# Optimization experiments

Hardware: AMD Instinct MI355X
Metric: run time of the kernel (lower is better)

The kernel has to match this reference:

```python
import jax, jax.numpy as jnp
import numpy as np

HIDDEN = 2048
N_HEADS = 16
N_KV_HEADS = 4
HEAD_DIM = HIDDEN // N_HEADS  # 128
BATCH = 1
SEQ = 2048
EPS = 1e-6


def _rms_norm(x, scale, eps=EPS):
    var = jnp.mean(jnp.square(x), axis=-1, keepdims=True)
    return x * jax.lax.rsqrt(var + eps) * scale


def _rotate_half(x):
    x1, x2 = jnp.split(x, 2, axis=-1)
    return jnp.concatenate((-x2, x1), axis=-1)


def setup_inputs() -> dict:
    key = jax.random.key(0)
    ks = jax.random.split(key, 8)
    hidden_states = jax.random.normal(ks[0], (BATCH, SEQ, HIDDEN), dtype=jnp.float32)
    # causal mask, broadcastable over [B, H, S, S]
    attention_mask = jnp.tril(jnp.ones((SEQ, SEQ), dtype=bool))[None, None, :, :]
    # standard RoPE tables, broadcastable against [B, S, H, D]
    inv_freq = 1.0 / (10000.0 ** (np.arange(0, HEAD_DIM, 2, dtype=np.float32) / HEAD_DIM))
    t = np.arange(SEQ, dtype=np.float32)
    freqs = np.outer(t, inv_freq)                      # [S, D/2]
    emb = np.concatenate([freqs, freqs], axis=-1)      # [S, D]
    cos = jnp.asarray(np.cos(emb))[:, None, :]         # [S, 1, D]
    sin = jnp.asarray(np.sin(emb))[:, None, :]
    s = 1.0 / np.sqrt(HIDDEN)
    Wq = jax.random.normal(ks[1], (HIDDEN, N_HEADS * HEAD_DIM), dtype=jnp.float32) * s
    Wk = jax.random.normal(ks[2], (HIDDEN, N_KV_HEADS * HEAD_DIM), dtype=jnp.float32) * s
    Wv = jax.random.normal(ks[3], (HIDDEN, N_KV_HEADS * HEAD_DIM), dtype=jnp.float32) * s
    Wo = jax.random.normal(ks[4], (HIDDEN, HIDDEN), dtype=jnp.float32) * s
    q_norm_scale = jnp.ones((HEAD_DIM,), dtype=jnp.float32)
    k_norm_scale = jnp.ones((HEAD_DIM,), dtype=jnp.float32)
    last_norm_scale = jnp.ones((HIDDEN,), dtype=jnp.float32)
    return {
        "hidden_states": hidden_states,
        "cos": cos,
        "sin": sin,
        "Wq": Wq,
        "Wk": Wk,
        "Wv": Wv,
        "Wo": Wo,
        "q_norm_scale": q_norm_scale,
        "k_norm_scale": k_norm_scale,
        "last_norm_scale": last_norm_scale,
        "attention_mask": attention_mask,
    }


def reference(hidden_states, cos, sin, Wq, Wk, Wv, Wo,
              q_norm_scale, k_norm_scale, last_norm_scale, attention_mask):
    B, S, _ = hidden_states.shape
    q = (hidden_states @ Wq).reshape(B, S, N_HEADS, HEAD_DIM)
    k = (hidden_states @ Wk).reshape(B, S, N_KV_HEADS, HEAD_DIM)
    v = (hidden_states @ Wv).reshape(B, S, N_KV_HEADS, HEAD_DIM)
    # per-head RMSNorm on Q/K
    q = _rms_norm(q, q_norm_scale)
    k = _rms_norm(k, k_norm_scale)
    # RoPE (cos/sin broadcast [S,1,D] -> [B,S,H,D])
    q = q * cos + _rotate_half(q) * sin
    k = k * cos + _rotate_half(k) * sin
    # GQA expansion
    groups = N_HEADS // N_KV_HEADS
    if groups > 1:
        k = jnp.repeat(k, groups, axis=2)
        v = jnp.repeat(v, groups, axis=2)
    out = jax.nn.dot_product_attention(q, k, v, mask=attention_mask)  # [B,S,H,D]
    out = out.reshape(B, S, HIDDEN) @ Wo
    return _rms_norm(out, last_norm_scale)
```

## Files before the change

### kernel.cpp

```cpp
#include <hip/hip_runtime.h>

typedef unsigned short u16;
typedef unsigned int u32;

#define S 2048
#define HID 2048
#define NH 16
#define NKV 4
#define D 128
#define QKVP 3072
#define QSCALE (0.08838834764831845f * 1.4426950408889634f)
#define NEG_INF -3.0e38f

typedef __attribute__((ext_vector_type(8))) short short8;
typedef __attribute__((ext_vector_type(4))) float f32x4;

__device__ __forceinline__ float bf2f(u16 u) {
  union { u32 i; float f; } c; c.i = ((u32)u) << 16; return c.f;
}
__device__ __forceinline__ u16 f2bf(float f) {
  union { float f; u32 i; } c; c.f = f;
  u32 x = c.i;
  u32 r = x + 0x7fffu + ((x >> 16) & 1u);
  return (u16)(r >> 16);
}

#if __has_builtin(__builtin_amdgcn_exp2f)
__device__ __forceinline__ float exp2_hw(float x) { return __builtin_amdgcn_exp2f(x); }
#else
__device__ __forceinline__ float exp2_hw(float x) { return exp2f(x); }
#endif

__device__ __forceinline__ u32 cvt_pk_bf16(float a, float b) {
  u32 r;
  asm("v_cvt_pk_bf16_f32 %0, %1, %2" : "=v"(r) : "v"(a), "v"(b));
  return r;
}

__device__ __forceinline__ void gload16(const u16* g, u16* l) {
  __builtin_amdgcn_global_load_lds(
      (const __attribute__((address_space(1))) u32*)g,
      (__attribute__((address_space(3))) u32*)l, 16, 0, 0);
}

__global__ __launch_bounds__(256) void k_cvt(const float* __restrict__ src,
                                             u16* __restrict__ dst) {
  int i = (blockIdx.x * 256 + threadIdx.x) * 8;
  float4 v0 = *(const float4*)(src + i);
  float4 v1 = *(const float4*)(src + i + 4);
  ushort4 w0, w1;
  w0.x = f2bf(v0.x); w0.y = f2bf(v0.y); w0.z = f2bf(v0.z); w0.w = f2bf(v0.w);
  w1.x = f2bf(v1.x); w1.y = f2bf(v1.y); w1.z = f2bf(v1.z); w1.w = f2bf(v1.w);
  *(ushort4*)(dst + i) = w0;
  *(ushort4*)(dst + i + 4) = w1;
}

__device__ __forceinline__ void transpose_body(const float* __restrict__ src,
                                               u16* __restrict__ dst,
                                               int N, int K, int nt, int kt,
                                               int t) {
  __shared__ float T[64][65];
#pragma unroll
  for (int it = 0; it < 4; ++it) {
    int r = it * 16 + (t >> 4), c = (t & 15) * 4;
    float4 v = *(const float4*)(src + (size_t)(kt + r) * N + nt + c);
    T[r][c] = v.x; T[r][c + 1] = v.y; T[r][c + 2] = v.z; T[r][c + 3] = v.w;
  }
  __syncthreads();
#pragma unroll
  for (int it = 0; it < 2; ++it) {
    int n = it * 32 + (t >> 3), k8 = (t & 7) * 8;
    ushort4 w0, w1;
    w0.x = f2bf(T[k8 + 0][n]); w0.y = f2bf(T[k8 + 1][n]);
    w0.z = f2bf(T[k8 + 2][n]); w0.w = f2bf(T[k8 + 3][n]);
    w1.x = f2bf(T[k8 + 4][n]); w1.y = f2bf(T[k8 + 5][n]);
    w1.z = f2bf(T[k8 + 6][n]); w1.w = f2bf(T[k8 + 7][n]);
    *(ushort4*)(dst + (size_t)(nt + n) * K + kt + k8) = w0;
    *(ushort4*)(dst + (size_t)(nt + n) * K + kt + k8 + 4) = w1;
  }
}

__global__ __launch_bounds__(256) void k_transpose(const float* __restrict__ src,
                                                   u16* __restrict__ dst,
                                                   int N, int K) {
  transpose_body(src, dst, N, K, blockIdx.x * 64, blockIdx.y * 64, threadIdx.x);
}

__global__ __launch_bounds__(256) void k_transpose_qkv(const float* __restrict__ Wq,
                                                       const float* __restrict__ Wk,
                                                       const float* __restrict__ Wv,
                                                       u16* __restrict__ WT) {
  const int bx = blockIdx.x;
  const float* src; u16* dst; int N, nt;
  if (bx < 32)      { src = Wq; dst = WT;                    N = 2048; nt = bx * 64; }
  else if (bx < 40) { src = Wk; dst = WT + 2048ull * 2048;   N = 512;  nt = (bx - 32) * 64; }
  else              { src = Wv; dst = WT + 2560ull * 2048;   N = 512;  nt = (bx - 40) * 64; }
  transpose_body(src, dst, N, 2048, nt, blockIdx.y * 64, threadIdx.x);
}

__global__ __launch_bounds__(256) void k_vt(const u16* __restrict__ QKV,
                                            u16* __restrict__ Vt) {
  __shared__ u16 T[64][66];
  const int t = threadIdx.x;
  const int s0 = blockIdx.x * 64, d0 = blockIdx.y * 64;
#pragma unroll
  for (int it = 0; it < 4; ++it) {
    int r = it * 16 + (t >> 4), c = (t & 15) * 4;
    ushort4 v = *(const ushort4*)(QKV + (size_t)(s0 + r) * QKVP + 2560 + d0 + c);
    T[r][c] = v.x; T[r][c + 1] = v.y; T[r][c + 2] = v.z; T[r][c + 3] = v.w;
  }
  __syncthreads();
#pragma unroll
  for (int it = 0; it < 4; ++it) {
    int dd = it * 16 + (t >> 4), sc = (t & 15) * 4;
    ushort4 w;
    w.x = T[sc + 0][dd]; w.y = T[sc + 1][dd];
    w.z = T[sc + 2][dd]; w.w = T[sc + 3][dd];
    *(ushort4*)(Vt + (size_t)(d0 + dd) * S + s0 + sc) = w;
  }
}

__global__ __launch_bounds__(256) void k_gemm_mfma(const u16* __restrict__ A,
                                                   const u16* __restrict__ BT,
                                                   void* __restrict__ Cout,
                                                   int N, int K, int out_bf16) {
  __shared__ __align__(16) u16 As[2][128 * 32];
  __shared__ __align__(16) u16 Bs[2][128 * 32];
  const int t = threadIdx.x, w = t >> 6, lane = t & 63;
  const int l15 = lane & 15, quad = lane >> 4;
  const int m0 = blockIdx.y * 128, n0 = blockIdx.x * 128;
  const int wr = w >> 1, wc = w & 1;

  const int sr = w * 16 + (lane >> 2);
  const int sk8 = (lane & 3) * 8;
  const u16* Ag0 = A + (size_t)(m0 + sr) * K + sk8;
  const u16* Ag1 = A + (size_t)(m0 + 64 + sr) * K + sk8;
  const u16* Bg0 = BT + (size_t)(n0 + sr) * K + sk8;
  const u16* Bg1 = BT + (size_t)(n0 + 64 + sr) * K + sk8;

  f32x4 acc[4][4];
#pragma unroll
  for (int i = 0; i < 4; ++i)
#pragma unroll
    for (int j = 0; j < 4; ++j) acc[i][j] = (f32x4){0.f, 0.f, 0.f, 0.f};

  auto STAGE = [&](int k0, int b) {
    gload16(Ag0 + k0, &As[b][w * 512]);
    gload16(Ag1 + k0, &As[b][2048 + w * 512]);
    gload16(Bg0 + k0, &Bs[b][w * 512]);
    gload16(Bg1 + k0, &Bs[b][2048 + w * 512]);
  };

  STAGE(0, 0);
  __syncthreads();
  int cur = 0;
  for (int k0 = 0; k0 < K; k0 += 32) {
    if (k0 + 32 < K) STAGE(k0 + 32, cur ^ 1);

    short8 af[4], bf[4];
#pragma unroll
    for (int i = 0; i < 4; ++i)
      af[i] = *(const short8*)&As[cur][(wr * 64 + i * 16 + l15) * 32 + quad * 8];
#pragma unroll
    for (int j = 0; j < 4; ++j)
      bf[j] = *(const short8*)&Bs[cur][(wc * 64 + j * 16 + l15) * 32 + quad * 8];
#pragma unroll
    for (int i = 0; i < 4; ++i)
#pragma unroll
      for (int j = 0; j < 4; ++j)
        acc[i][j] = __builtin_amdgcn_mfma_f32_16x16x32_bf16(af[i], bf[j], acc[i][j], 0, 0, 0);

    __syncthreads();
    cur ^= 1;
  }

  if (out_bf16) {
    u16* C = (u16*)Cout;
#pragma unroll
    for (int i = 0; i < 4; ++i)
#pragma unroll
      for (int j = 0; j < 4; ++j) {
        int col = n0 + wc * 64 + j * 16 + l15;
#pragma unroll
        for (int r = 0; r < 4; ++r)
          C[(size_t)(m0 + wr * 64 + i * 16 + quad * 4 + r) * N + col] = f2bf(acc[i][j][r]);
      }
  } else {
    float* C = (float*)Cout;
#pragma unroll
    for (int i = 0; i < 4; ++i)
#pragma unroll
      for (int j = 0; j < 4; ++j) {
        int col = n0 + wc * 64 + j * 16 + l15;
#pragma unroll
        for (int r = 0; r < 4; ++r)
          C[(size_t)(m0 + wr * 64 + i * 16 + quad * 4 + r) * N + col] = acc[i][j][r];
      }
  }
}

__global__ __launch_bounds__(128) void k_norm_rope(u16* __restrict__ QKV,
                                                   const float* __restrict__ qsc,
                                                   const float* __restrict__ ksc,
                                                   const float* __restrict__ cosp,
                                                   const float* __restrict__ sinp) {
  const int s = blockIdx.x, hh = blockIdx.y, d = threadIdx.x;
  u16* row; const float* sc; float scale;
  if (hh < NH) { row = QKV + (size_t)s * QKVP + hh * D;            sc = qsc; scale = QSCALE; }
  else         { row = QKV + (size_t)s * QKVP + 2048 + (hh - NH) * D; sc = ksc; scale = 1.0f; }
  float x = bf2f(row[d]);
  float v = x * x;
#pragma unroll
  for (int o = 32; o; o >>= 1) v += __shfl_xor(v, o, 64);
  __shared__ float red[2];
  if ((d & 63) == 0) red[d >> 6] = v;
  __syncthreads();
  float var = (red[0] + red[1]) * (1.0f / 128.0f);
  float rinv = rsqrtf(var + 1e-6f) * scale;
  float xn = x * rinv * sc[d];
  __shared__ float sh[D];
  sh[d] = xn;
  __syncthreads();
  float rot = (d < 64) ? -sh[d + 64] : sh[d - 64];
  row[d] = f2bf(xn * cosp[s * D + d] + rot * sinp[s * D + d]);
}

#define KP 128
#define PTP 72

__global__ __launch_bounds__(256) void k_flash(const u16* __restrict__ QKV,
                                               const u16* __restrict__ Vt,
                                               u16* __restrict__ O) {
  const int h = blockIdx.y, g = h >> 2;
  const int qt = (h < 8) ? (31 - (int)blockIdx.x) : (int)blockIdx.x;
  const int t = threadIdx.x;
  const int w = t >> 6, lane = t & 63, l15 = lane & 15, quad = lane >> 4;

  __shared__ __align__(16) u16 Klds[2][64 * KP];
  __shared__ __align__(16) u16 Vlds[128 * 64];
  __shared__ __align__(16) u16 Pt[4][16 * PTP];

  const int qbase = qt * 64 + w * 16;
  const int qrow = qbase + l15;

  short8 qf[4];
  {
    const u16* qp = QKV + (size_t)qrow * QKVP + h * D + quad * 8;
#pragma unroll
    for (int c = 0; c < 4; ++c) qf[c] = *(const short8*)(qp + c * 32);
  }

  float m = NEG_INF, l = 0.f;
  f32x4 oacc[8];
#pragma unroll
  for (int nc = 0; nc < 8; ++nc) oacc[nc] = (f32x4){0.f, 0.f, 0.f, 0.f};

  const int nt = qt + 1;
  const int dd = t >> 3, cc = t & 7;

  auto KLOAD = [&](int j0, int b) {
#pragma unroll
    for (int it = 0; it < 4; ++it) {
      int rl = w * 16 + it * 4 + quad;
      int gchunk = (lane & 15) ^ (rl & 7);
      const u16* gp = QKV + (size_t)(j0 + rl) * QKVP + 2048 + g * D + gchunk * 8;
      gload16(gp, &Klds[b][(w * 16 + it * 4) * KP]);
    }
  };
  auto VLOAD = [&](int j0, uint4* vr) {
#pragma unroll
    for (int it = 0; it < 4; ++it)
      vr[it] = *(const uint4*)(Vt + (size_t)(g * D + dd + it * 32) * S + j0 + cc * 8);
  };
  auto VWRITE = [&](uint4* vr) {
#pragma unroll
    for (int it = 0; it < 4; ++it) {
      int d = dd + it * 32;
      *(uint4*)&Vlds[d * 64 + ((cc ^ (d & 7)) * 8)] = vr[it];
    }
  };
  auto COMPUTE = [&](int jt, int b) {
    const int j0 = jt * 64;
    f32x4 sa[4];
#pragma unroll
    for (int sub = 0; sub < 4; ++sub) {
      f32x4 acc = {0.f, 0.f, 0.f, 0.f};
#pragma unroll
      for (int c = 0; c < 4; ++c) {
        int ch = (c * 4 + quad) ^ (l15 & 7);
        short8 kf = *(const short8*)&Klds[b][(sub * 16 + l15) * KP + ch * 8];
        acc = __builtin_amdgcn_mfma_f32_16x16x32_bf16(kf, qf[c], acc, 0, 0, 0);
      }
      sa[sub] = acc;
    }
    if (jt == nt - 1) {
#pragma unroll
      for (int sub = 0; sub < 4; ++sub) {
        int keyb = j0 + sub * 16 + quad * 4;
#pragma unroll
        for (int r = 0; r < 4; ++r)
          if (keyb + r > qrow) sa[sub][r] = NEG_INF;
      }
    }
    float tmax = sa[0][0];
#pragma unroll
    for (int sub = 0; sub < 4; ++sub)
#pragma unroll
      for (int r = 0; r < 4; ++r) tmax = fmaxf(tmax, sa[sub][r]);
    tmax = fmaxf(tmax, __shfl_xor(tmax, 16, 64));
    tmax = fmaxf(tmax, __shfl_xor(tmax, 32, 64));
    float mn = fmaxf(m, tmax);
    float alpha = exp2_hw(m - mn);
    m = mn;
    float rs = 0.f;
#pragma unroll
    for (int sub = 0; sub < 4; ++sub) {
      float p0 = exp2_hw(sa[sub][0] - m);
      float p1 = exp2_hw(sa[sub][1] - m);
      float p2 = exp2_hw(sa[sub][2] - m);
      float p3 = exp2_hw(sa[sub][3] - m);
      rs += (p0 + p1) + (p2 + p3);
      u32 lo = cvt_pk_bf16(p0, p1);
      u32 hi = cvt_pk_bf16(p2, p3);
      *(uint2*)&Pt[w][l15 * PTP + sub * 16 + quad * 4] = make_uint2(lo, hi);
    }
    rs += __shfl_xor(rs, 16, 64);
    rs += __shfl_xor(rs, 32, 64);
    l = l * alpha + rs;
#pragma unroll
    for (int nc = 0; nc < 8; ++nc) {
      oacc[nc][0] *= alpha; oacc[nc][1] *= alpha;
      oacc[nc][2] *= alpha; oacc[nc][3] *= alpha;
    }
#pragma unroll
    for (int kc = 0; kc < 2; ++kc) {
      short8 pf = *(const short8*)&Pt[w][l15 * PTP + kc * 32 + quad * 8];
#pragma unroll
      for (int nc = 0; nc < 8; ++nc) {
        int d = nc * 16 + l15;
        short8 vf = *(const short8*)&Vlds[d * 64 + (((kc * 4 + quad) ^ (d & 7)) * 8)];
        oacc[nc] = __builtin_amdgcn_mfma_f32_16x16x32_bf16(vf, pf, oacc[nc], 0, 0, 0);
      }
    }
  };

  uint4 vrA[4], vrB[4];
  KLOAD(0, 0);
  VLOAD(0, vrA);
  for (int jt = 0; jt < nt; jt += 2) {
    __syncthreads();
    VWRITE(vrA);
    __syncthreads();
    if (jt + 1 < nt) { KLOAD((jt + 1) * 64, 1); VLOAD((jt + 1) * 64, vrB); }
    COMPUTE(jt, 0);
    if (jt + 1 < nt) {
      __syncthreads();
      VWRITE(vrB);
      __syncthreads();
      if (jt + 2 < nt) { KLOAD((jt + 2) * 64, 0); VLOAD((jt + 2) * 64, vrA); }
      COMPUTE(jt + 1, 1);
    }
  }

  float inv = 1.0f / l;
  u16* orow = O + (size_t)qrow * HID + h * D;
#pragma unroll
  for (int nc = 0; nc < 8; ++nc) {
    ushort4 wv;
    wv.x = f2bf(oacc[nc][0] * inv); wv.y = f2bf(oacc[nc][1] * inv);
    wv.z = f2bf(oacc[nc][2] * inv); wv.w = f2bf(oacc[nc][3] * inv);
    *(ushort4*)(orow + nc * 16 + quad * 4) = wv;
  }
}

__device__ __forceinline__ float blockSum256(float v, float* red, int t) {
#pragma unroll
  for (int o = 32; o; o >>= 1) v += __shfl_xor(v, o, 64);
  if ((t & 63) == 0) red[t >> 6] = v;
  __syncthreads();
  v = red[0] + red[1] + red[2] + red[3];
  __syncthreads();
  return v;
}

__global__ __launch_bounds__(256) void k_fnorm(const float* __restrict__ X,
                                               const float* __restrict__ sc,
                                               float* __restrict__ out) {
  const int s = blockIdx.x, t = threadIdx.x;
  const float* row = X + (size_t)s * HID;
  float4 r0 = *(const float4*)(row + t * 8);
  float4 r1 = *(const float4*)(row + t * 8 + 4);
  float x[8] = {r0.x, r0.y, r0.z, r0.w, r1.x, r1.y, r1.z, r1.w};
  float ss = 0.f;
#pragma unroll
  for (int ii = 0; ii < 8; ++ii) ss += x[ii] * x[ii];
  __shared__ float red[4];
  float tot = blockSum256(ss, red, t);
  float rinv = rsqrtf(tot * (1.0f / 2048.0f) + 1e-6f);
  float4 s0 = *(const float4*)(sc + t * 8);
  float4 s1 = *(const float4*)(sc + t * 8 + 4);
  float4 w0 = make_float4(x[0] * rinv * s0.x, x[1] * rinv * s0.y,
                          x[2] * rinv * s0.z, x[3] * rinv * s0.w);
  float4 w1 = make_float4(x[4] * rinv * s1.x, x[5] * rinv * s1.y,
                          x[6] * rinv * s1.z, x[7] * rinv * s1.w);
  *(float4*)(out + (size_t)s * HID + t * 8) = w0;
  *(float4*)(out + (size_t)s * HID + t * 8 + 4) = w1;
}

extern "C" void kernel_launch(void* const* d_in, const int* in_sizes, int n_in,
                              void* d_out, int out_size, void* d_ws, size_t ws_size,
                              hipStream_t stream) {
  const float* hidden = (const float*)d_in[0];
  const float* cosp   = (const float*)d_in[1];
  const float* sinp   = (const float*)d_in[2];
  const float* Wq     = (const float*)d_in[3];
  const float* Wk     = (const float*)d_in[4];
  const float* Wv     = (const float*)d_in[5];
  const float* Wo     = (const float*)d_in[6];
  const float* qsc    = (const float*)d_in[7];
  const float* ksc    = (const float*)d_in[8];
  const float* lsc    = (const float*)d_in[9];
  float* out = (float*)d_out;

  char* ws = (char*)d_ws;
  u16*   Hb  = (u16*)(ws);
  u16*   WoT = (u16*)(ws);
  u16*   WT  = (u16*)(ws + (8ull << 20));
  u16*   An  = (u16*)(ws + (8ull << 20));
  u16*   QKV = (u16*)(ws + (20ull << 20));
  float* Ob  = (float*)(ws + (20ull << 20));
  u16*   Vtb = (u16*)(ws + (32ull << 20));

  k_cvt<<<S * HID / (256 * 8), 256, 0, stream>>>(hidden, Hb);
  k_transpose_qkv<<<dim3(48, 32), 256, 0, stream>>>(Wq, Wk, Wv, WT);
  k_gemm_mfma<<<dim3(24, 16), 256, 0, stream>>>(Hb, WT, QKV, QKVP, 2048, 1);
  k_transpose<<<dim3(32, 32), 256, 0, stream>>>(Wo, WoT, 2048, 2048);
  k_norm_rope<<<dim3(S, NH + NKV), 128, 0, stream>>>(QKV, qsc, ksc, cosp, sinp);
  k_vt<<<dim3(32, 8), 256, 0, stream>>>(QKV, Vtb);
  k_flash<<<dim3(32, NH), 256, 0, stream>>>(QKV, Vtb, An);
  k_gemm_mfma<<<dim3(16, 16), 256, 0, stream>>>(An, WoT, Ob, 2048, 2048, 0);
  k_fnorm<<<S, 256, 0, stream>>>(Ob, lsc, out);
}
```

Before: 321.9 us.

## Load V fragments directly from global into registers and skip rescaling lazily

The flash kernel no longer stages V through LDS. Each wave reads its V^T MFMA fragments straight from global memory into registers, split into two halves issued around the QK^T MFMAs, and the loop drops to one barrier per tile. The online-softmax rescale of the output accumulator is also skipped unless the running max grows by more than 8 (in log2 units) for some lane. This removes LDS writes and barriers, but every wave now fetches the full V tile from global/L2 on its own (4x redundant reads per block) and register pressure rises.

```diff
diff --git a/kernel.cpp b/kernel.cpp
--- a/kernel.cpp
+++ b/kernel.cpp
@@ -237,7 +237,6 @@
   const int w = t >> 6, lane = t & 63, l15 = lane & 15, quad = lane >> 4;
 
   __shared__ __align__(16) u16 Klds[2][64 * KP];
-  __shared__ __align__(16) u16 Vlds[128 * 64];
   __shared__ __align__(16) u16 Pt[4][16 * PTP];
 
   const int qbase = qt * 64 + w * 16;
@@ -256,7 +255,6 @@
   for (int nc = 0; nc < 8; ++nc) oacc[nc] = (f32x4){0.f, 0.f, 0.f, 0.f};
 
   const int nt = qt + 1;
-  const int dd = t >> 3, cc = t & 7;
 
   auto KLOAD = [&](int j0, int b) {
 #pragma unroll
@@ -267,20 +265,21 @@
       gload16(gp, &Klds[b][(w * 16 + it * 4) * KP]);
     }
   };
-  auto VLOAD = [&](int j0, uint4* vr) {
-#pragma unroll
-    for (int it = 0; it < 4; ++it)
-      vr[it] = *(const uint4*)(Vt + (size_t)(g * D + dd + it * 32) * S + j0 + cc * 8);
-  };
-  auto VWRITE = [&](uint4* vr) {
-#pragma unroll
-    for (int it = 0; it < 4; ++it) {
-      int d = dd + it * 32;
-      *(uint4*)&Vlds[d * 64 + ((cc ^ (d & 7)) * 8)] = vr[it];
-    }
-  };
-  auto COMPUTE = [&](int jt, int b) {
+
+  KLOAD(0, 0);
+  for (int jt = 0; jt < nt; ++jt) {
+    const int b = jt & 1;
+    __syncthreads();
+    if (jt + 1 < nt) KLOAD((jt + 1) * 64, b ^ 1);
+
     const int j0 = jt * 64;
+    const u16* vbase = Vt + (size_t)g * D * S + j0;
+
+    short8 vf0[8];
+#pragma unroll
+    for (int nc = 0; nc < 8; ++nc)
+      vf0[nc] = *(const short8*)(vbase + (size_t)(nc * 16 + l15) * S + quad * 8);
+
     f32x4 sa[4];
 #pragma unroll
     for (int sub = 0; sub < 4; ++sub) {
@@ -293,6 +292,12 @@
       }
       sa[sub] = acc;
     }
+
+    short8 vf1[8];
+#pragma unroll
+    for (int nc = 0; nc < 8; ++nc)
+      vf1[nc] = *(const short8*)(vbase + (size_t)(nc * 16 + l15) * S + 32 + quad * 8);
+
     if (jt == nt - 1) {
 #pragma unroll
       for (int sub = 0; sub < 4; ++sub) {
@@ -302,6 +307,7 @@
           if (keyb + r > qrow) sa[sub][r] = NEG_INF;
       }
     }
+
     float tmax = sa[0][0];
 #pragma unroll
     for (int sub = 0; sub < 4; ++sub)
@@ -309,9 +315,17 @@
       for (int r = 0; r < 4; ++r) tmax = fmaxf(tmax, sa[sub][r]);
     tmax = fmaxf(tmax, __shfl_xor(tmax, 16, 64));
     tmax = fmaxf(tmax, __shfl_xor(tmax, 32, 64));
-    float mn = fmaxf(m, tmax);
-    float alpha = exp2_hw(m - mn);
-    m = mn;
+    if (jt == 0 || !__all(tmax - m <= 8.f)) {
+      float mn = (jt == 0) ? tmax : fmaxf(m, tmax);
+      float alpha = (jt == 0) ? 0.f : exp2_hw(m - mn);
+      m = mn;
+      l *= alpha;
+#pragma unroll
+      for (int nc = 0; nc < 8; ++nc) {
+        oacc[nc][0] *= alpha; oacc[nc][1] *= alpha;
+        oacc[nc][2] *= alpha; oacc[nc][3] *= alpha;
+      }
+    }
     float rs = 0.f;
 #pragma unroll
     for (int sub = 0; sub < 4; ++sub) {
@@ -326,39 +340,17 @@
     }
     rs += __shfl_xor(rs, 16, 64);
     rs += __shfl_xor(rs, 32, 64);
-    l = l * alpha + rs;
-#pragma unroll
-    for (int nc = 0; nc < 8; ++nc) {
-      oacc[nc][0] *= alpha; oacc[nc][1] *= alpha;
-      oacc[nc][2] *= alpha; oacc[nc][3] *= alpha;
-    }
-#pragma unroll
-    for (int kc = 0; kc < 2; ++kc) {
-      short8 pf = *(const short8*)&Pt[w][l15 * PTP + kc * 32 + quad * 8];
-#pragma unroll
-      for (int nc = 0; nc < 8; ++nc) {
-        int d = nc * 16 + l15;
-        short8 vf = *(const short8*)&Vlds[d * 64 + (((kc * 4 + quad) ^ (d & 7)) * 8)];
-        oacc[nc] = __builtin_amdgcn_mfma_f32_16x16x32_bf16(vf, pf, oacc[nc], 0, 0, 0);
-      }
-    }
-  };
-
-  uint4 vrA[4], vrB[4];
-  KLOAD(0, 0);
-  VLOAD(0, vrA);
-  for (int jt = 0; jt < nt; jt += 2) {
-    __syncthreads();
-    VWRITE(vrA);
-    __syncthreads();
-    if (jt + 1 < nt) { KLOAD((jt + 1) * 64, 1); VLOAD((jt + 1) * 64, vrB); }
-    COMPUTE(jt, 0);
-    if (jt + 1 < nt) {
-      __syncthreads();
-      VWRITE(vrB);
-      __syncthreads();
-      if (jt + 2 < nt) { KLOAD((jt + 2) * 64, 0); VLOAD((jt + 2) * 64, vrA); }
-      COMPUTE(jt + 1, 1);
+    l += rs;
+
+    {
+      short8 pf0 = *(const short8*)&Pt[w][l15 * PTP + quad * 8];
+      short8 pf1 = *(const short8*)&Pt[w][l15 * PTP + 32 + quad * 8];
+#pragma unroll
+      for (int nc = 0; nc < 8; ++nc)
+        oacc[nc] = __builtin_amdgcn_mfma_f32_16x16x32_bf16(vf0[nc], pf0, oacc[nc], 0, 0, 0);
+#pragma unroll
+      for (int nc = 0; nc < 8; ++nc)
+        oacc[nc] = __builtin_amdgcn_mfma_f32_16x16x32_bf16(vf1[nc], pf1, oacc[nc], 0, 0, 0);
     }
   }
 
```

New measurement: 333.0 us. 3.5% more time.

## Retile GEMM to 128x64 blocks with K=64 stages and XOR-swizzled LDS

Applied to the files above, without the earlier changes.

The MFMA GEMM moves from 128x128 output tiles with a K step of 32 to 128x64 tiles with a K step of 64. LDS chunks are XOR-swizzled to avoid bank conflicts, and each wave now owns 32 rows across the full 64 columns. The grid doubles so the QKV and output projections launch more blocks across the CUs, and there are half as many barriers per K. In exchange, each block reuses fewer A/B loads, so global traffic per output goes up, and each thread holds fewer accumulators.

```diff
diff --git a/kernel.cpp b/kernel.cpp
--- a/kernel.cpp
+++ b/kernel.cpp
@@ -124,51 +124,56 @@
                                                    const u16* __restrict__ BT,
                                                    void* __restrict__ Cout,
                                                    int N, int K, int out_bf16) {
-  __shared__ __align__(16) u16 As[2][128 * 32];
-  __shared__ __align__(16) u16 Bs[2][128 * 32];
+  __shared__ __align__(16) u16 As[2][128 * 64];
+  __shared__ __align__(16) u16 Bs[2][64 * 64];
   const int t = threadIdx.x, w = t >> 6, lane = t & 63;
   const int l15 = lane & 15, quad = lane >> 4;
-  const int m0 = blockIdx.y * 128, n0 = blockIdx.x * 128;
-  const int wr = w >> 1, wc = w & 1;
-
-  const int sr = w * 16 + (lane >> 2);
-  const int sk8 = (lane & 3) * 8;
-  const u16* Ag0 = A + (size_t)(m0 + sr) * K + sk8;
-  const u16* Ag1 = A + (size_t)(m0 + 64 + sr) * K + sk8;
-  const u16* Bg0 = BT + (size_t)(n0 + sr) * K + sk8;
-  const u16* Bg1 = BT + (size_t)(n0 + 64 + sr) * K + sk8;
-
-  f32x4 acc[4][4];
-#pragma unroll
-  for (int i = 0; i < 4; ++i)
+  const int m0 = blockIdx.y * 128, n0 = blockIdx.x * 64;
+
+  const int srow = lane >> 3;
+  const int schunk = (lane & 7) ^ srow;
+  const u16* Agb = A + (size_t)(m0 + w * 8 + srow) * K + schunk * 8;
+  const u16* Bgb = BT + (size_t)(n0 + w * 8 + srow) * K + schunk * 8;
+
+  f32x4 acc[2][4];
+#pragma unroll
+  for (int i = 0; i < 2; ++i)
 #pragma unroll
     for (int j = 0; j < 4; ++j) acc[i][j] = (f32x4){0.f, 0.f, 0.f, 0.f};
 
   auto STAGE = [&](int k0, int b) {
-    gload16(Ag0 + k0, &As[b][w * 512]);
-    gload16(Ag1 + k0, &As[b][2048 + w * 512]);
-    gload16(Bg0 + k0, &Bs[b][w * 512]);
-    gload16(Bg1 + k0, &Bs[b][2048 + w * 512]);
+#pragma unroll
+    for (int it = 0; it < 4; ++it)
+      gload16(Agb + (size_t)it * 32 * K + k0, &As[b][(w * 8 + it * 32) * 64]);
+#pragma unroll
+    for (int it = 0; it < 2; ++it)
+      gload16(Bgb + (size_t)it * 32 * K + k0, &Bs[b][(w * 8 + it * 32) * 64]);
   };
 
   STAGE(0, 0);
   __syncthreads();
   int cur = 0;
-  for (int k0 = 0; k0 < K; k0 += 32) {
-    if (k0 + 32 < K) STAGE(k0 + 32, cur ^ 1);
-
-    short8 af[4], bf[4];
-#pragma unroll
-    for (int i = 0; i < 4; ++i)
-      af[i] = *(const short8*)&As[cur][(wr * 64 + i * 16 + l15) * 32 + quad * 8];
-#pragma unroll
-    for (int j = 0; j < 4; ++j)
-      bf[j] = *(const short8*)&Bs[cur][(wc * 64 + j * 16 + l15) * 32 + quad * 8];
-#pragma unroll
-    for (int i = 0; i < 4; ++i)
+  for (int k0 = 0; k0 < K; k0 += 64) {
+    if (k0 + 64 < K) STAGE(k0 + 64, cur ^ 1);
+
+    short8 af[2][2], bf[4][2];
+#pragma unroll
+    for (int k2 = 0; k2 < 2; ++k2) {
+      int ch = (k2 * 4 + quad) ^ (l15 & 7);
+#pragma unroll
+      for (int i = 0; i < 2; ++i)
+        af[i][k2] = *(const short8*)&As[cur][(w * 32 + i * 16 + l15) * 64 + ch * 8];
 #pragma unroll
       for (int j = 0; j < 4; ++j)
-        acc[i][j] = __builtin_amdgcn_mfma_f32_16x16x32_bf16(af[i], bf[j], acc[i][j], 0, 0, 0);
+        bf[j][k2] = *(const short8*)&Bs[cur][(j * 16 + l15) * 64 + ch * 8];
+    }
+#pragma unroll
+    for (int k2 = 0; k2 < 2; ++k2)
+#pragma unroll
+      for (int i = 0; i < 2; ++i)
+#pragma unroll
+        for (int j = 0; j < 4; ++j)
+          acc[i][j] = __builtin_amdgcn_mfma_f32_16x16x32_bf16(af[i][k2], bf[j][k2], acc[i][j], 0, 0, 0);
 
     __syncthreads();
     cur ^= 1;
@@ -177,24 +182,24 @@
   if (out_bf16) {
     u16* C = (u16*)Cout;
 #pragma unroll
-    for (int i = 0; i < 4; ++i)
+    for (int i = 0; i < 2; ++i)
 #pragma unroll
       for (int j = 0; j < 4; ++j) {
-        int col = n0 + wc * 64 + j * 16 + l15;
+        int col = n0 + j * 16 + l15;
 #pragma unroll
         for (int r = 0; r < 4; ++r)
-          C[(size_t)(m0 + wr * 64 + i * 16 + quad * 4 + r) * N + col] = f2bf(acc[i][j][r]);
+          C[(size_t)(m0 + w * 32 + i * 16 + quad * 4 + r) * N + col] = f2bf(acc[i][j][r]);
       }
   } else {
     float* C = (float*)Cout;
 #pragma unroll
-    for (int i = 0; i < 4; ++i)
+    for (int i = 0; i < 2; ++i)
 #pragma unroll
       for (int j = 0; j < 4; ++j) {
-        int col = n0 + wc * 64 + j * 16 + l15;
+        int col = n0 + j * 16 + l15;
 #pragma unroll
         for (int r = 0; r < 4; ++r)
-          C[(size_t)(m0 + wr * 64 + i * 16 + quad * 4 + r) * N + col] = acc[i][j][r];
+          C[(size_t)(m0 + w * 32 + i * 16 + quad * 4 + r) * N + col] = acc[i][j][r];
       }
   }
 }
@@ -433,11 +438,11 @@
 
   k_cvt<<<S * HID / (256 * 8), 256, 0, stream>>>(hidden, Hb);
   k_transpose_qkv<<<dim3(48, 32), 256, 0, stream>>>(Wq, Wk, Wv, WT);
-  k_gemm_mfma<<<dim3(24, 16), 256, 0, stream>>>(Hb, WT, QKV, QKVP, 2048, 1);
+  k_gemm_mfma<<<dim3(48, 16), 256, 0, stream>>>(Hb, WT, QKV, QKVP, 2048, 1);
   k_transpose<<<dim3(32, 32), 256, 0, stream>>>(Wo, WoT, 2048, 2048);
   k_norm_rope<<<dim3(S, NH + NKV), 128, 0, stream>>>(QKV, qsc, ksc, cosp, sinp);
   k_vt<<<dim3(32, 8), 256, 0, stream>>>(QKV, Vtb);
   k_flash<<<dim3(32, NH), 256, 0, stream>>>(QKV, Vtb, An);
-  k_gemm_mfma<<<dim3(16, 16), 256, 0, stream>>>(An, WoT, Ob, 2048, 2048, 0);
+  k_gemm_mfma<<<dim3(32, 16), 256, 0, stream>>>(An, WoT, Ob, 2048, 2048, 0);
   k_fnorm<<<S, 256, 0, stream>>>(Ob, lsc, out);
 }
```

Measured after the change: 306.8 us. -4.7%, faster.
